# Kernel optimization log

Hardware: AMD Instinct MI355X
Metric: run time of the kernel (lower is better)

## Reference

```python
import jax, jax.numpy as jnp
import numpy as np


def setup_inputs() -> dict:
    key = jax.random.key(0)
    k1, k2, k3 = jax.random.split(key, 3)
    B, S, H, E = 8, 4096, 2048, 64
    hidden_states = jax.random.normal(k1, (B, S, H), dtype=jnp.float32)
    # kaiming_uniform-ish scale for the gate weight [E, H]
    weight = jax.random.normal(k2, (E, H), dtype=jnp.float32) * (1.0 / np.sqrt(H))
    # load-balancing biases are small perturbations of the softmax scores
    expert_biases = jax.random.normal(k3, (E,), dtype=jnp.float32) * 0.01
    return {"hidden_states": hidden_states, "weight": weight,
            "expert_biases": expert_biases, "top_k": 8}


def reference(hidden_states, weight, expert_biases, top_k):
    B, S, H = hidden_states.shape
    x = hidden_states.reshape(-1, H).astype(jnp.float32)          # [T, H], T = B*S
    logits = jnp.einsum('th,eh->te', x, weight.astype(jnp.float32))  # [T, E]
    scores = jax.nn.softmax(logits, axis=-1)                      # fp32 softmax
    bias_scores = scores + expert_biases[None, :]                 # bias-adjusted routing
    _, topk_indices = jax.lax.top_k(bias_scores, top_k)           # [T, K] (sorted; set equals torch sorted=False)
    topk_weights = jnp.take_along_axis(scores, topk_indices, axis=1)  # gather original probs
    if top_k > 1:  # norm_topk_prob=True
        topk_weights = topk_weights / (topk_weights.sum(-1, keepdims=True) + 1e-20)
    return (topk_indices.astype(jnp.int32),
            topk_weights.astype(hidden_states.dtype))
```

## Files before the change

kernel.cpp:

```cpp
#include <hip/hip_runtime.h>
#include <math.h>

#define Hdim   2048
#define HF4    512
#define MARGIN 2e-5f
#define CAPF   16384
#define PROBE0 1237
#define PROBE1 20011

#define WS_FCNT  0
#define WS_BAD   4
#define WS_PROBE 64
#define WS_FLIST 1024
#define WS_WH    (128*1024)
#define WS_WL    (384*1024)
#define WS_NEED  (640*1024)

typedef float f32x4 __attribute__((ext_vector_type(4)));
typedef short bf8   __attribute__((ext_vector_type(8)));

typedef const __attribute__((address_space(1))) unsigned int ga_u32;
typedef __attribute__((address_space(3))) unsigned int la_u32;
__device__ __forceinline__ void gload16(const void* g, void* l) {
  __builtin_amdgcn_global_load_lds((ga_u32*)g, (la_u32*)l, 16, 0, 0);
}

__device__ __forceinline__ short bf_hi(float v, float& rem) {
  const unsigned u  = __builtin_bit_cast(unsigned, v);
  const unsigned uh = u & 0xffff0000u;
  rem = v - __builtin_bit_cast(float, uh);
  return (short)(u >> 16);
}
__device__ __forceinline__ short bf_rne(float v) {
  const unsigned u = __builtin_bit_cast(unsigned, v);
  return (short)((u + 0x7fffu + ((u >> 16) & 1u)) >> 16);
}

__global__ __launch_bounds__(256) void gate_prep(
    const float* __restrict__ wgt, short* __restrict__ WH, short* __restrict__ WL)
{
  const int f  = blockIdx.x * 256 + threadIdx.x;
  const int c  = f >> 11;
  const int et = (f >> 9) & 3;
  const int l  = (f >> 3) & 63;
  const int j  = f & 7;
  const int e  = et * 16 + (l & 15);
  const int k  = c * 32 + (l >> 4) * 8 + j;
  const float w = wgt[(size_t)e * Hdim + k];
  float r; const short h = bf_hi(w, r);
  WH[f] = h; WL[f] = bf_rne(r);
}

__global__ __launch_bounds__(256, 3) void gate_main(
    const float* __restrict__ x, const short* __restrict__ WH,
    const short* __restrict__ WL, const float* __restrict__ eb,
    float* __restrict__ out, int* __restrict__ fcnt, int* __restrict__ flist,
    float* __restrict__ probelg, int T)
{
  __shared__ __align__(16) char smem[49152];
  const int t    = threadIdx.x;
  const int wv   = t >> 6;
  const int ln   = t & 63;
  const int tokb = blockIdx.x * 64;
  const int tb   = tokb + wv * 16;

  const int l3 = ln >> 3;
  const int sx = (ln & 7) ^ (l3 & 6);
  const float* xsrc0 = x + (size_t)(tokb + (wv * 2 + 0) * 8 + l3) * Hdim + sx * 4;
  const float* xsrc1 = x + (size_t)(tokb + (wv * 2 + 1) * 8 + l3) * Hdim + sx * 4;
  const short* whsrc = WH + wv * 512 + ln * 8;
  const short* wlsrc = WL + wv * 512 + ln * 8;

  const int Aoff = (wv * 16 + (ln & 15)) * 32 + ((((ln >> 4) * 2) ^ (ln & 6)) * 4);

  f32x4 acc[4];
  #pragma unroll
  for (int et = 0; et < 4; ++et) acc[et] = (f32x4)0.f;

#define STAGE(kk, SL) {                                                    \
    char* sl_ = smem + ((SL) * 16384);                                     \
    gload16(xsrc0 + (kk) * 32, sl_ + (wv * 2 + 0) * 1024);                 \
    gload16(xsrc1 + (kk) * 32, sl_ + (wv * 2 + 1) * 1024);                 \
    gload16(whsrc + (size_t)(kk) * 2048, sl_ + 8192  + wv * 1024);         \
    gload16(wlsrc + (size_t)(kk) * 2048, sl_ + 12288 + wv * 1024);         \
  }

#define STEP(kk, SC, SN, WAITN) {                                          \
    if ((kk) < 63) STAGE((kk) + 1, SN);                                    \
    asm volatile("s_waitcnt vmcnt(" #WAITN ")" ::: "memory");              \
    __builtin_amdgcn_s_barrier();                                          \
    const char*  sl_ = smem + ((SC) * 16384);                              \
    const float* xs_ = (const float*)sl_;                                  \
    f32x4 Af0 = *(const f32x4*)(xs_ + Aoff);                               \
    f32x4 Af1 = *(const f32x4*)(xs_ + Aoff + 4);                           \
    const short* bh_ = (const short*)(sl_ + 8192)  + ln * 8;               \
    const short* bl_ = (const short*)(sl_ + 12288) + ln * 8;               \
    bf8 Bh0 = *(const bf8*)(bh_);                                          \
    bf8 Bh1 = *(const bf8*)(bh_ + 512);                                    \
    bf8 Bh2 = *(const bf8*)(bh_ + 1024);                                   \
    bf8 Bh3 = *(const bf8*)(bh_ + 1536);                                   \
    bf8 Bl0 = *(const bf8*)(bl_);                                          \
    bf8 Bl1 = *(const bf8*)(bl_ + 512);                                    \
    bf8 Bl2 = *(const bf8*)(bl_ + 1024);                                   \
    bf8 Bl3 = *(const bf8*)(bl_ + 1536);                                   \
    asm volatile("s_waitcnt lgkmcnt(0)" ::: "memory");                     \
    __builtin_amdgcn_sched_barrier(0);                                     \
    bf8 ah, al;                                                            \
    _Pragma("unroll")                                                      \
    for (int j = 0; j < 4; ++j) {                                          \
      float r_;                                                            \
      ah[j]     = bf_hi(Af0[j], r_);  al[j]     = bf_rne(r_);              \
      ah[j + 4] = bf_hi(Af1[j], r_);  al[j + 4] = bf_rne(r_);              \
    }                                                                      \
    acc[0] = __builtin_amdgcn_mfma_f32_16x16x32_bf16(ah, Bh0, acc[0], 0, 0, 0); \
    acc[0] = __builtin_amdgcn_mfma_f32_16x16x32_bf16(ah, Bl0, acc[0], 0, 0, 0); \
    acc[0] = __builtin_amdgcn_mfma_f32_16x16x32_bf16(al, Bh0, acc[0], 0, 0, 0); \
    acc[0] = __builtin_amdgcn_mfma_f32_16x16x32_bf16(al, Bl0, acc[0], 0, 0, 0); \
    acc[1] = __builtin_amdgcn_mfma_f32_16x16x32_bf16(ah, Bh1, acc[1], 0, 0, 0); \
    acc[1] = __builtin_amdgcn_mfma_f32_16x16x32_bf16(ah, Bl1, acc[1], 0, 0, 0); \
    acc[1] = __builtin_amdgcn_mfma_f32_16x16x32_bf16(al, Bh1, acc[1], 0, 0, 0); \
    acc[1] = __builtin_amdgcn_mfma_f32_16x16x32_bf16(al, Bl1, acc[1], 0, 0, 0); \
    acc[2] = __builtin_amdgcn_mfma_f32_16x16x32_bf16(ah, Bh2, acc[2], 0, 0, 0); \
    acc[2] = __builtin_amdgcn_mfma_f32_16x16x32_bf16(ah, Bl2, acc[2], 0, 0, 0); \
    acc[2] = __builtin_amdgcn_mfma_f32_16x16x32_bf16(al, Bh2, acc[2], 0, 0, 0); \
    acc[2] = __builtin_amdgcn_mfma_f32_16x16x32_bf16(al, Bl2, acc[2], 0, 0, 0); \
    acc[3] = __builtin_amdgcn_mfma_f32_16x16x32_bf16(ah, Bh3, acc[3], 0, 0, 0); \
    acc[3] = __builtin_amdgcn_mfma_f32_16x16x32_bf16(ah, Bl3, acc[3], 0, 0, 0); \
    acc[3] = __builtin_amdgcn_mfma_f32_16x16x32_bf16(al, Bh3, acc[3], 0, 0, 0); \
    acc[3] = __builtin_amdgcn_mfma_f32_16x16x32_bf16(al, Bl3, acc[3], 0, 0, 0); \
  }

  STAGE(0, 0);
  #pragma unroll 1
  for (int ks = 0; ks < 63; ks += 3) {
    STEP(ks,     0, 1, 4);
    STEP(ks + 1, 1, 2, 4);
    STEP(ks + 2, 2, 0, 4);
  }
  STEP(63, 0, 0, 0);
#undef STEP
#undef STAGE

  const int c = ln & 15, g = ln >> 4;
  float bias4[4];
  #pragma unroll
  for (int et = 0; et < 4; ++et) bias4[et] = eb[et * 16 + c];

  #pragma unroll
  for (int r = 0; r < 4; ++r) {
    const int gt = tb + g * 4 + r;
    const float z0 = acc[0][r], z1 = acc[1][r], z2 = acc[2][r], z3 = acc[3][r];
    if (gt == PROBE0) { probelg[c]      = z0; probelg[16 + c] = z1;
                        probelg[32 + c] = z2; probelg[48 + c] = z3; }
    if (gt == PROBE1) { probelg[64 + c]  = z0; probelg[80 + c]  = z1;
                        probelg[96 + c]  = z2; probelg[112 + c] = z3; }
    float m = fmaxf(fmaxf(z0, z1), fmaxf(z2, z3));
    #pragma unroll
    for (int off = 1; off < 16; off <<= 1) m = fmaxf(m, __shfl_xor(m, off, 64));
    const float p0 = expf(z0 - m), p1 = expf(z1 - m);
    const float p2 = expf(z2 - m), p3 = expf(z3 - m);
    float Zs = (p0 + p1) + (p2 + p3);
    #pragma unroll
    for (int off = 1; off < 16; off <<= 1) Zs += __shfl_xor(Zs, off, 64);
    const float inv = 1.f / Zs;
    const float s0 = p0 * inv, s1 = p1 * inv, s2 = p2 * inv, s3 = p3 * inv;
    float b0 = s0 + bias4[0], b1 = s1 + bias4[1];
    float b2 = s2 + bias4[2], b3 = s3 + bias4[3];
    float prev = 0.f, gmin = 1e30f, mys = 0.f;
    int myi = 0;
    #pragma unroll
    for (int r9 = 0; r9 < 9; ++r9) {
      float v = b0; int ie = 0;
      if (b1 > v) { v = b1; ie = 1; }
      if (b2 > v) { v = b2; ie = 2; }
      if (b3 > v) { v = b3; ie = 3; }
      int idx = ie * 16 + c;
      #pragma unroll
      for (int off = 1; off < 16; off <<= 1) {
        const float ov = __shfl_xor(v, off, 64);
        const int   oi = __shfl_xor(idx, off, 64);
        if (ov > v || (ov == v && oi < idx)) { v = ov; idx = oi; }
      }
      if (r9) gmin = fminf(gmin, prev - v);
      prev = v;
      if (r9 < 8) {
        const int oe = idx >> 4, oc = idx & 15;
        const float cand = oe == 0 ? s0 : oe == 1 ? s1 : oe == 2 ? s2 : s3;
        const float sv = __shfl(cand, g * 16 + oc, 64);
        if (c == r9) { myi = idx; mys = sv; }
        if (c == oc) {
          if (oe == 0) b0 = -1e30f;
          else if (oe == 1) b1 = -1e30f;
          else if (oe == 2) b2 = -1e30f;
          else b3 = -1e30f;
        }
      }
    }
    float wsum = (c < 8) ? mys : 0.f;
    #pragma unroll
    for (int off = 1; off < 16; off <<= 1) wsum += __shfl_xor(wsum, off, 64);
    if (c < 8) {
      out[(size_t)gt * 8 + c] = (float)myi;
      out[(size_t)T * 8 + (size_t)gt * 8 + c] = mys / (wsum + 1e-20f);
    }
    if (c == 0 && gmin < MARGIN) {
      const int pos = atomicAdd(fcnt, 1);
      if (pos < CAPF) flist[pos] = gt;
    }
  }
}

__global__ __launch_bounds__(256) void gate_check(
    const float* __restrict__ x, const float* __restrict__ wgt,
    const float* __restrict__ probelg, const int* __restrict__ fcnt,
    int* __restrict__ allbad)
{
  __shared__ float part[64][4];
  const int p = blockIdx.x;
  const int P = p ? PROBE1 : PROBE0;
  const int t = threadIdx.x, e = t >> 2, q = t & 3;
  const float4* xr = (const float4*)(x + (size_t)P * Hdim);
  const float4* wr = (const float4*)(wgt + (size_t)e * Hdim);
  float a = 0.f, b = 0.f, c = 0.f, d = 0.f;
  for (int i = 0; i < 128; ++i) {
    const int f4 = i * 4 + q;
    const float4 xv = xr[f4], wv = wr[f4];
    a = fmaf(xv.x, wv.x, a); b = fmaf(xv.y, wv.y, b);
    c = fmaf(xv.z, wv.z, c); d = fmaf(xv.w, wv.w, d);
  }
  part[e][q] = (a + b) + (c + d);
  __syncthreads();
  if (q == 0) {
    const float z = part[e][0] + part[e][1] + part[e][2] + part[e][3];
    if (fabsf(z - probelg[p * 64 + e]) > 0.05f) *allbad = 1;
  }
  if (t == 0 && p == 0 && *fcnt > CAPF) *allbad = 1;
}

__global__ __launch_bounds__(256) void gate_fix(
    const float* __restrict__ x, const float* __restrict__ wgt,
    const float* __restrict__ eb, float* __restrict__ out,
    const int* __restrict__ fcnt, const int* __restrict__ flist,
    const int* __restrict__ allbad, int T)
{
  __shared__ float4 xl[4 * HF4];
  __shared__ double part[4][64][4];
  __shared__ int tks[4];
  const int bad = *allbad;
  int n = bad ? T : *fcnt;
  if (n <= 0) return;
  if (!bad && n > CAPF) n = CAPF;
  const int nb = (n + 3) >> 2;
  const int t = threadIdx.x;
  for (int b = blockIdx.x; b < nb; b += gridDim.x) {
    if (t < 4) {
      const int li = b * 4 + t;
      const int ci = li < n ? li : n - 1;
      tks[t] = bad ? ci : flist[ci];
    }
    __syncthreads();
    {
      const int m = t >> 6, l2 = t & 63;
      const float4* src = (const float4*)x + (size_t)tks[m] * HF4;
      #pragma unroll
      for (int ii = 0; ii < 8; ++ii) xl[m * HF4 + ii * 64 + l2] = src[ii * 64 + l2];
    }
    __syncthreads();
    const int e = t >> 2, q = t & 3;
    double acc[4] = {0.0, 0.0, 0.0, 0.0};
    const float4* w4 = (const float4*)wgt + (size_t)e * HF4;
    for (int c = 0; c < 128; ++c) {
      const int f4 = c * 4 + q;
      const float4 wvv = w4[f4];
      #pragma unroll
      for (int m = 0; m < 4; ++m) {
        const float4 xv = xl[m * HF4 + f4];
        acc[m] += (double)xv.x * (double)wvv.x + (double)xv.y * (double)wvv.y
                + (double)xv.z * (double)wvv.z + (double)xv.w * (double)wvv.w;
      }
    }
    #pragma unroll
    for (int m = 0; m < 4; ++m) part[m][e][q] = acc[m];
    __syncthreads();
    {
      const int m = t >> 6, ln = t & 63;
      const double z = part[m][ln][0] + part[m][ln][1] + part[m][ln][2] + part[m][ln][3];
      double mx = z;
      #pragma unroll
      for (int off = 32; off; off >>= 1) mx = fmax(mx, __shfl_xor(mx, off, 64));
      const double p = exp(z - mx);
      double Zs = p;
      #pragma unroll
      for (int off = 32; off; off >>= 1) Zs += __shfl_xor(Zs, off, 64);
      const double sco = p / Zs;
      double bsw = sco + (double)eb[ln];
      double mys = 0.0;
      int myi = 0;
      #pragma unroll
      for (int r = 0; r < 8; ++r) {
        double v = bsw;
        int idx = ln;
        #pragma unroll
        for (int off = 32; off; off >>= 1) {
          const double ov = __shfl_xor(v, off, 64);
          const int   oi = __shfl_xor(idx, off, 64);
          if (ov > v || (ov == v && oi < idx)) { v = ov; idx = oi; }
        }
        const double sv = __shfl(sco, idx, 64);
        if (ln == r)  { myi = idx; mys = sv; }
        if (ln == idx) bsw = -1.0e300;
      }
      double wsum = (ln < 8) ? mys : 0.0;
      #pragma unroll
      for (int off = 32; off; off >>= 1) wsum += __shfl_xor(wsum, off, 64);
      const int gt = tks[m];
      if (ln < 8) {
        out[(size_t)gt * 8 + ln] = (float)myi;
        out[(size_t)T * 8 + (size_t)gt * 8 + ln] = (float)(mys / (wsum + 1e-20));
      }
    }
    __syncthreads();
  }
}

extern "C" void kernel_launch(void* const* d_in, const int* in_sizes, int n_in,
                              void* d_out, int out_size, void* d_ws, size_t ws_size,
                              hipStream_t stream) {
  const float* x   = (const float*)d_in[0];
  const float* wgt = (const float*)d_in[1];
  const float* eb  = (const float*)d_in[2];
  float* out = (float*)d_out;
  const int T = in_sizes[0] / Hdim;
  char* ws = (char*)d_ws;
  int*   fcnt    = (int*)(ws + WS_FCNT);
  int*   bad     = (int*)(ws + WS_BAD);
  float* probelg = (float*)(ws + WS_PROBE);
  int*   flist   = (int*)(ws + WS_FLIST);
  short* WH      = (short*)(ws + WS_WH);
  short* WL      = (short*)(ws + WS_WL);

  if (ws_size < WS_NEED) {
    hipMemsetAsync(ws, 0, 8, stream);
    hipMemsetAsync(ws + WS_BAD, 1, 1, stream);
    hipLaunchKernelGGL(gate_fix, dim3(256), dim3(256), 0, stream,
                       x, wgt, eb, out, fcnt, flist, bad, T);
    return;
  }
  hipMemsetAsync(ws, 0, 8, stream);
  hipLaunchKernelGGL(gate_prep, dim3(512), dim3(256), 0, stream, wgt, WH, WL);
  hipLaunchKernelGGL(gate_main, dim3(T / 64), dim3(256), 0, stream,
                     x, WH, WL, eb, out, fcnt, flist, probelg, T);
  hipLaunchKernelGGL(gate_check, dim3(2), dim3(256), 0, stream,
                     x, wgt, probelg, fcnt, bad);
  hipLaunchKernelGGL(gate_fix, dim3(256), dim3(256), 0, stream,
                     x, wgt, eb, out, fcnt, flist, bad, T);
}
```

Baseline: 141.8 us.

## Load activations directly to registers and deepen weight LDS pipeline

Activation tiles now go straight from global memory into registers with inline dwordx4 loads, double-buffered across steps, instead of being staged through LDS. Only the bf16 hi/lo weight tiles still pass through LDS, now in a four-slot ring with two stages prefetched ahead. The hi/lo split of x is done before the barrier, and the MFMA block runs at raised wave priority. LDS per block shrinks, but the launch bound drops from 3 to 2 blocks per SIMD to leave more registers, which may reduce latency hiding. The inline asm vmcnt counting must match the number of loads in flight exactly.

```diff
diff --git a/kernel.cpp b/kernel.cpp
--- a/kernel.cpp
+++ b/kernel.cpp
@@ -51,50 +51,74 @@
   WH[f] = h; WL[f] = bf_rne(r);
 }
 
-__global__ __launch_bounds__(256, 3) void gate_main(
+__global__ __launch_bounds__(256, 2) void gate_main(
     const float* __restrict__ x, const short* __restrict__ WH,
     const short* __restrict__ WL, const float* __restrict__ eb,
     float* __restrict__ out, int* __restrict__ fcnt, int* __restrict__ flist,
     float* __restrict__ probelg, int T)
 {
-  __shared__ __align__(16) char smem[49152];
+  __shared__ __align__(16) char smem[32768];
   const int t    = threadIdx.x;
   const int wv   = t >> 6;
   const int ln   = t & 63;
-  const int tokb = blockIdx.x * 64;
-  const int tb   = tokb + wv * 16;
-
-  const int l3 = ln >> 3;
-  const int sx = (ln & 7) ^ (l3 & 6);
-  const float* xsrc0 = x + (size_t)(tokb + (wv * 2 + 0) * 8 + l3) * Hdim + sx * 4;
-  const float* xsrc1 = x + (size_t)(tokb + (wv * 2 + 1) * 8 + l3) * Hdim + sx * 4;
-  const short* whsrc = WH + wv * 512 + ln * 8;
-  const short* wlsrc = WL + wv * 512 + ln * 8;
-
-  const int Aoff = (wv * 16 + (ln & 15)) * 32 + ((((ln >> 4) * 2) ^ (ln & 6)) * 4);
+  const int tb   = blockIdx.x * 64 + wv * 16;
+
+  const char* xq = (const char*)(x + (size_t)(tb + (ln & 15)) * Hdim + (ln >> 4) * 8);
+  const short* whq = WH + t * 8;
+  const short* wlq = WL + t * 8;
 
   f32x4 acc[4];
   #pragma unroll
   for (int et = 0; et < 4; ++et) acc[et] = (f32x4)0.f;
 
-#define STAGE(kk, SL) {                                                    \
-    char* sl_ = smem + ((SL) * 16384);                                     \
-    gload16(xsrc0 + (kk) * 32, sl_ + (wv * 2 + 0) * 1024);                 \
-    gload16(xsrc1 + (kk) * 32, sl_ + (wv * 2 + 1) * 1024);                 \
-    gload16(whsrc + (size_t)(kk) * 2048, sl_ + 8192  + wv * 1024);         \
-    gload16(wlsrc + (size_t)(kk) * 2048, sl_ + 12288 + wv * 1024);         \
-  }
-
-#define STEP(kk, SC, SN, WAITN) {                                          \
-    if ((kk) < 63) STAGE((kk) + 1, SN);                                    \
-    asm volatile("s_waitcnt vmcnt(" #WAITN ")" ::: "memory");              \
+  f32x4 xE0, xE1, xO0, xO1;
+
+#define XLOAD(D0, D1, OA, OB)                                              \
+  asm volatile("global_load_dwordx4 %0, %2, off offset:" #OA "\n\t"        \
+               "global_load_dwordx4 %1, %2, off offset:" #OB               \
+               : "=v"(D0), "=v"(D1) : "v"(xq) : "memory")
+
+#define WSTAGE(SLOT, KOFF) {                                               \
+    gload16(whq + (KOFF), smem + (SLOT) * 8192 + wv * 1024);               \
+    gload16(wlq + (KOFF), smem + (SLOT) * 8192 + 4096 + wv * 1024); }
+
+#define SPLIT(X0, X1) {                                                    \
+    _Pragma("unroll")                                                      \
+    for (int j = 0; j < 4; ++j) { float r_;                                \
+      ah[j]     = bf_hi(X0[j], r_);  al[j]     = bf_rne(r_);               \
+      ah[j + 4] = bf_hi(X1[j], r_);  al[j + 4] = bf_rne(r_); } }
+
+#define MF16()                                                                    \
+    __builtin_amdgcn_s_setprio(1);                                                \
+    acc[0] = __builtin_amdgcn_mfma_f32_16x16x32_bf16(ah, Bh0, acc[0], 0, 0, 0);   \
+    acc[0] = __builtin_amdgcn_mfma_f32_16x16x32_bf16(ah, Bl0, acc[0], 0, 0, 0);   \
+    acc[0] = __builtin_amdgcn_mfma_f32_16x16x32_bf16(al, Bh0, acc[0], 0, 0, 0);   \
+    acc[0] = __builtin_amdgcn_mfma_f32_16x16x32_bf16(al, Bl0, acc[0], 0, 0, 0);   \
+    acc[1] = __builtin_amdgcn_mfma_f32_16x16x32_bf16(ah, Bh1, acc[1], 0, 0, 0);   \
+    acc[1] = __builtin_amdgcn_mfma_f32_16x16x32_bf16(ah, Bl1, acc[1], 0, 0, 0);   \
+    acc[1] = __builtin_amdgcn_mfma_f32_16x16x32_bf16(al, Bh1, acc[1], 0, 0, 0);   \
+    acc[1] = __builtin_amdgcn_mfma_f32_16x16x32_bf16(al, Bl1, acc[1], 0, 0, 0);   \
+    acc[2] = __builtin_amdgcn_mfma_f32_16x16x32_bf16(ah, Bh2, acc[2], 0, 0, 0);   \
+    acc[2] = __builtin_amdgcn_mfma_f32_16x16x32_bf16(ah, Bl2, acc[2], 0, 0, 0);   \
+    acc[2] = __builtin_amdgcn_mfma_f32_16x16x32_bf16(al, Bh2, acc[2], 0, 0, 0);   \
+    acc[2] = __builtin_amdgcn_mfma_f32_16x16x32_bf16(al, Bl2, acc[2], 0, 0, 0);   \
+    acc[3] = __builtin_amdgcn_mfma_f32_16x16x32_bf16(ah, Bh3, acc[3], 0, 0, 0);   \
+    acc[3] = __builtin_amdgcn_mfma_f32_16x16x32_bf16(ah, Bl3, acc[3], 0, 0, 0);   \
+    acc[3] = __builtin_amdgcn_mfma_f32_16x16x32_bf16(al, Bh3, acc[3], 0, 0, 0);   \
+    acc[3] = __builtin_amdgcn_mfma_f32_16x16x32_bf16(al, Bl3, acc[3], 0, 0, 0);   \
+    __builtin_amdgcn_s_setprio(0);
+
+#define STEP(SCUR, XI, WI, XS0, XS1, VM) {                                 \
+    XI; WI;                                                                \
+    asm volatile("s_waitcnt vmcnt(" #VM ")" ::: "memory");                 \
+    __builtin_amdgcn_sched_barrier(0);                                     \
+    bf8 ah, al;                                                            \
+    SPLIT(XS0, XS1);                                                       \
+    asm volatile("" ::: "memory");                                         \
     __builtin_amdgcn_s_barrier();                                          \
-    const char*  sl_ = smem + ((SC) * 16384);                              \
-    const float* xs_ = (const float*)sl_;                                  \
-    f32x4 Af0 = *(const f32x4*)(xs_ + Aoff);                               \
-    f32x4 Af1 = *(const f32x4*)(xs_ + Aoff + 4);                           \
-    const short* bh_ = (const short*)(sl_ + 8192)  + ln * 8;               \
-    const short* bl_ = (const short*)(sl_ + 12288) + ln * 8;               \
+    asm volatile("" ::: "memory");                                         \
+    const short* bh_ = (const short*)(smem + (SCUR) * 8192) + ln * 8;      \
+    const short* bl_ = bh_ + 2048;                                         \
     bf8 Bh0 = *(const bf8*)(bh_);                                          \
     bf8 Bh1 = *(const bf8*)(bh_ + 512);                                    \
     bf8 Bh2 = *(const bf8*)(bh_ + 1024);                                   \
@@ -103,43 +127,30 @@
     bf8 Bl1 = *(const bf8*)(bl_ + 512);                                    \
     bf8 Bl2 = *(const bf8*)(bl_ + 1024);                                   \
     bf8 Bl3 = *(const bf8*)(bl_ + 1536);                                   \
-    asm volatile("s_waitcnt lgkmcnt(0)" ::: "memory");                     \
-    __builtin_amdgcn_sched_barrier(0);                                     \
-    bf8 ah, al;                                                            \
-    _Pragma("unroll")                                                      \
-    for (int j = 0; j < 4; ++j) {                                          \
-      float r_;                                                            \
-      ah[j]     = bf_hi(Af0[j], r_);  al[j]     = bf_rne(r_);              \
-      ah[j + 4] = bf_hi(Af1[j], r_);  al[j + 4] = bf_rne(r_);              \
-    }                                                                      \
-    acc[0] = __builtin_amdgcn_mfma_f32_16x16x32_bf16(ah, Bh0, acc[0], 0, 0, 0); \
-    acc[0] = __builtin_amdgcn_mfma_f32_16x16x32_bf16(ah, Bl0, acc[0], 0, 0, 0); \
-    acc[0] = __builtin_amdgcn_mfma_f32_16x16x32_bf16(al, Bh0, acc[0], 0, 0, 0); \
-    acc[0] = __builtin_amdgcn_mfma_f32_16x16x32_bf16(al, Bl0, acc[0], 0, 0, 0); \
-    acc[1] = __builtin_amdgcn_mfma_f32_16x16x32_bf16(ah, Bh1, acc[1], 0, 0, 0); \
-    acc[1] = __builtin_amdgcn_mfma_f32_16x16x32_bf16(ah, Bl1, acc[1], 0, 0, 0); \
-    acc[1] = __builtin_amdgcn_mfma_f32_16x16x32_bf16(al, Bh1, acc[1], 0, 0, 0); \
-    acc[1] = __builtin_amdgcn_mfma_f32_16x16x32_bf16(al, Bl1, acc[1], 0, 0, 0); \
-    acc[2] = __builtin_amdgcn_mfma_f32_16x16x32_bf16(ah, Bh2, acc[2], 0, 0, 0); \
-    acc[2] = __builtin_amdgcn_mfma_f32_16x16x32_bf16(ah, Bl2, acc[2], 0, 0, 0); \
-    acc[2] = __builtin_amdgcn_mfma_f32_16x16x32_bf16(al, Bh2, acc[2], 0, 0, 0); \
-    acc[2] = __builtin_amdgcn_mfma_f32_16x16x32_bf16(al, Bl2, acc[2], 0, 0, 0); \
-    acc[3] = __builtin_amdgcn_mfma_f32_16x16x32_bf16(ah, Bh3, acc[3], 0, 0, 0); \
-    acc[3] = __builtin_amdgcn_mfma_f32_16x16x32_bf16(ah, Bl3, acc[3], 0, 0, 0); \
-    acc[3] = __builtin_amdgcn_mfma_f32_16x16x32_bf16(al, Bh3, acc[3], 0, 0, 0); \
-    acc[3] = __builtin_amdgcn_mfma_f32_16x16x32_bf16(al, Bl3, acc[3], 0, 0, 0); \
-  }
-
-  STAGE(0, 0);
+    MF16();                                                                \
+  }
+
+  XLOAD(xE0, xE1, 0, 16);
+  WSTAGE(0, 0);
+  WSTAGE(1, 2048);
+
   #pragma unroll 1
-  for (int ks = 0; ks < 63; ks += 3) {
-    STEP(ks,     0, 1, 4);
-    STEP(ks + 1, 1, 2, 4);
-    STEP(ks + 2, 2, 0, 4);
-  }
-  STEP(63, 0, 0, 0);
+  for (int ks = 0; ks < 60; ks += 4) {
+    STEP(0, XLOAD(xO0, xO1, 128, 144), WSTAGE(2, 4096),  xE0, xE1, 6);
+    STEP(1, XLOAD(xE0, xE1, 256, 272), WSTAGE(3, 6144),  xO0, xO1, 6);
+    STEP(2, XLOAD(xO0, xO1, 384, 400), WSTAGE(0, 8192),  xE0, xE1, 6);
+    STEP(3, XLOAD(xE0, xE1, 512, 528), WSTAGE(1, 10240), xO0, xO1, 6);
+    xq += 512; whq += 8192; wlq += 8192;
+  }
+  STEP(0, XLOAD(xO0, xO1, 128, 144), WSTAGE(2, 4096), xE0, xE1, 6);
+  STEP(1, XLOAD(xE0, xE1, 256, 272), WSTAGE(3, 6144), xO0, xO1, 6);
+  STEP(2, XLOAD(xO0, xO1, 384, 400), ,                xE0, xE1, 4);
+  STEP(3, ,                          ,                xO0, xO1, 0);
 #undef STEP
-#undef STAGE
+#undef MF16
+#undef SPLIT
+#undef WSTAGE
+#undef XLOAD
 
   const int c = ln & 15, g = ln >> 4;
   float bias4[4];
```

Result: slower. 144.7 us (+2.0%).
